# Optimization experiments

Hardware: AMD Instinct MI355X
Metric: run time of the kernel (lower is better)

## Reference

```python
import jax, jax.numpy as jnp
import numpy as np

N_SITE, D, PHYS, W = 40, 128, 2, 8  # sites, MPS bond dim, physical dim, MPO bond dim


def setup_inputs() -> dict:
    key = jax.random.key(0)
    k1, k2 = jax.random.split(key)
    # scale so 40-step transfer-matrix products stay O(1) in float32
    M = jax.random.normal(k1, (N_SITE, D, PHYS, D), jnp.float32) * (D * PHYS) ** -0.5
    H = jax.random.normal(k2, (N_SITE, W, W, PHYS, PHYS), jnp.float32) * (W * PHYS * PHYS) ** -0.5
    return {"M": M, "H": H}


def _energy(M, H):
    # <M|H|M> via left-to-right environment sweep. L has shape (D_bra, w, D_ket).
    L0 = jnp.zeros((D, W, D), M.dtype).at[0, 0, 0].set(1.0)  # open left boundary

    def step(L, mh):
        m, h = mh  # m: (a,i,p) bond,phys,bond ; h: (w,x,i,j) mpo-bond,mpo-bond,phys-out,phys-in
        T = jnp.einsum('awb,aip->wbip', L, m)      # absorb bra tensor (real, so no conj)
        T = jnp.einsum('wbip,wxij->bpxj', T, h)    # absorb MPO tensor
        L = jnp.einsum('bpxj,bjq->pxq', T, m)      # absorb ket tensor
        return L, None

    L, _ = jax.lax.scan(step, L0, (M, H))
    return L[0, W - 1, 0]  # open right boundary (MPO right boundary = last index)


def _norm(M):
    # <M|M> via transfer-matrix sweep. N has shape (D_bra, D_ket); stays PSD.
    N0 = jnp.zeros((D, D), M.dtype).at[0, 0].set(1.0)

    def step(N, m):
        T = jnp.einsum('ab,aip->bip', N, m)
        N = jnp.einsum('bip,biq->pq', T, m)
        return N, None

    N, _ = jax.lax.scan(step, N0, M)
    return N[0, 0]


def reference(M, H):
    EPS = 0.0
    NORM_LIM = 10000.0
    energy = _energy(M, H)
    norm = _norm(M)
    loss = energy / (norm + EPS)  # torch.real is identity for real dtype
    reg = jax.nn.relu(norm - NORM_LIM)
    return (energy, norm, loss, reg)
```

## Files before the change

kernel.cpp:

```cpp
#include <hip/hip_runtime.h>


#define D 128
#define W 8
#define NS 40
#define NPAIR 20
#define HALF2 10
#define MSZ (D * 2 * D)
#define HSZ (W * W * 2 * 2)
#define M2SZ (D * 4 * D)
#define H2SZ (W * W * 4 * 4)
#define LSZ (D * W * D)
#define NSZ (D * D)
#define T2SZ (D * W * D * 4)
#define TNSZ (4 * D * D)

#define OFF_M2 0
#define OFF_MR2 (OFF_M2 + NPAIR * M2SZ)
#define OFF_H2 (OFF_MR2 + HALF2 * M2SZ)
#define OFF_HR2 (OFF_H2 + NPAIR * H2SZ)
#define OFF_LL (OFF_HR2 + HALF2 * H2SZ)
#define OFF_LR (OFF_LL + LSZ)
#define OFF_NL (OFF_LR + LSZ)
#define OFF_NR (OFF_NL + NSZ)
#define OFF_T2L (OFF_NR + NSZ)
#define OFF_T2R (OFF_T2L + T2SZ)
#define OFF_TNL (OFF_T2R + T2SZ)
#define OFF_TNR (OFF_TNL + TNSZ)
#define OFF_PART (OFF_TNR + TNSZ)
#define OFF_PARTN (OFF_PART + 128)

__global__ __launch_bounds__(256) void k_prep1(const float* __restrict__ Min,
                                               const float* __restrict__ Hin,
                                               float* __restrict__ ws) {
    __shared__ float As[32 * 34];
    __shared__ float Bs[32 * 68];
    int bid = blockIdx.x, t = threadIdx.x;
    if (bid < 640) {
        int m = bid >> 5, tile = bid & 31;
        int r0 = (tile & 7) * 32, c0 = (tile >> 3) * 64;
        const float* A = Min + (2 * m) * MSZ;
        const float* B = Min + (2 * m + 1) * MSZ;
        float* C = ws + OFF_M2 + m * M2SZ;
        int ty = t >> 4, tx = t & 15;
        float a00 = 0, a01 = 0, a02 = 0, a03 = 0;
        float a10 = 0, a11 = 0, a12 = 0, a13 = 0;
        for (int c = 0; c < 4; ++c) {
            int k0 = c * 32;
            __syncthreads();
            {
                int rr = t >> 3, kq = t & 7;
                int row = r0 + rr;
                const float4 v = *(const float4*)&A[(row >> 1) * 256 + (row & 1) * 128 + k0 + kq * 4];
                float* dst = &As[kq * 136 + rr];
                dst[0] = v.x; dst[34] = v.y; dst[68] = v.z; dst[102] = v.w;
            }
#pragma unroll
            for (int u = 0; u < 2; ++u) {
                int e = u * 256 + t;
                int kk = e >> 4, cq = e & 15;
                const float4 v = *(const float4*)&B[(k0 + kk) * 256 + c0 + cq * 4];
                *(float4*)&Bs[kk * 68 + cq * 4] = v;
            }
            __syncthreads();
#pragma unroll 8
            for (int kk = 0; kk < 32; ++kk) {
                float2 av = *(float2*)&As[kk * 34 + 2 * ty];
                float4 bv = *(float4*)&Bs[kk * 68 + 4 * tx];
                a00 += av.x * bv.x; a01 += av.x * bv.y; a02 += av.x * bv.z; a03 += av.x * bv.w;
                a10 += av.y * bv.x; a11 += av.y * bv.y; a12 += av.y * bv.z; a13 += av.y * bv.w;
            }
        }
        int r = r0 + 2 * ty, cc = c0 + 4 * tx;
        int a = r >> 1, i2 = cc >> 7, cd = cc & 127;
        float4 v0; v0.x = a00; v0.y = a01; v0.z = a02; v0.w = a03;
        float4 v1; v1.x = a10; v1.y = a11; v1.z = a12; v1.w = a13;
        *(float4*)&C[a * 512 + (0 * 2 + i2) * 128 + cd] = v0;
        *(float4*)&C[a * 512 + (1 * 2 + i2) * 128 + cd] = v1;
    } else {
        for (int idx = t; idx < NPAIR * H2SZ; idx += 256) {
            int m = idx >> 10, r = idx & 1023;
            int w = r >> 7, x = (r >> 4) & 7, I = (r >> 2) & 3, J = r & 3;
            int i1 = I >> 1, i2 = I & 1, j1 = J >> 1, j2 = J & 1;
            const float* Ha = Hin + (2 * m) * HSZ;
            const float* Hb = Hin + (2 * m + 1) * HSZ;
            float s = 0.f;
#pragma unroll
            for (int v = 0; v < 8; ++v)
                s += Ha[w * 32 + v * 4 + i1 * 2 + j1] * Hb[v * 32 + x * 4 + i2 * 2 + j2];
            ws[OFF_H2 + idx] = s;
        }
    }
}

#define PR_MR (HALF2 * M2SZ)
#define PR_HR (PR_MR + HALF2 * H2SZ)
#define PR_TOT (PR_HR + 2 * LSZ + 2 * NSZ)
__global__ __launch_bounds__(256) void k_prep2(float* __restrict__ ws) {
    for (int idx = blockIdx.x * 256 + threadIdx.x; idx < PR_TOT; idx += gridDim.x * 256) {
        if (idx < PR_MR) {
            int kr = idx >> 16, r = idx & 65535;
            int a = r >> 9, I = (r >> 7) & 3, p = r & 127;
            ws[OFF_MR2 + idx] = ws[OFF_M2 + (19 - kr) * M2SZ + p * 512 + I * 128 + a];
        } else if (idx < PR_HR) {
            int e = idx - PR_MR;
            int kr = e >> 10, r = e & 1023;
            int w = r >> 7, x = (r >> 4) & 7, lo = r & 15;
            ws[OFF_HR2 + e] = ws[OFF_H2 + (19 - kr) * H2SZ + x * 128 + w * 16 + lo];
        } else {
            int e = idx - PR_HR;
            int off; float v = 0.f;
            if (e < LSZ)            { off = OFF_LL + e; if (e == 0) v = 1.f; }
            else if (e < 2 * LSZ)   { int r = e - LSZ; off = OFF_LR + r; if (r == (W - 1) * D) v = 1.f; }
            else if (e < 2 * LSZ + NSZ) { int r = e - 2 * LSZ; off = OFF_NL + r; if (r == 0) v = 1.f; }
            else                    { int r = e - 2 * LSZ - NSZ; off = OFF_NR + r; if (r == 0) v = 1.f; }
            ws[off] = v;
        }
    }
}

__global__ __launch_bounds__(512) void k_A2(float* __restrict__ ws, int k) {
    __shared__ __align__(16) float sm[17920];
    int bid = blockIdx.x, t = threadIdx.x;
    int z = t >> 8, tl = t & 255;
    if (bid < 128) {
        int side = bid >> 6;
        int eb = bid & 63;
        int b0 = (eb & 7) * 16;
        int p0 = (eb >> 3) * 16;
        const float* Lsrc = ws + (side ? OFF_LR : OFF_LL);
        const float* m2 = ws + (side ? OFF_MR2 : OFF_M2) + k * M2SZ;
        const float* h2 = ws + (side ? OFF_HR2 : OFF_H2) + k * H2SZ;
        float* T2 = ws + (side ? OFF_T2R : OFF_T2L);
        float* Ls = sm + z * 6400;
        float* ms = sm + 12800 + z * 2048;
        float* hs = sm + 16896;
#pragma unroll
        for (int u = 0; u < 2; ++u) {
            int e = u * 512 + t;
            int w = e >> 7, I = (e >> 5) & 3, x = (e >> 2) & 7, J = e & 3;
            hs[e] = h2[w * 128 + x * 16 + I * 4 + J];
        }
        int b_l = tl & 15, p_l = tl >> 4;
        float acc[8][4];
#pragma unroll
        for (int w = 0; w < 8; ++w)
#pragma unroll
            for (int I = 0; I < 4; ++I) acc[w][I] = 0.f;
        int la[4], lw[4], lb[4], maa[2], mI[2], mpq[2];
#pragma unroll
        for (int u = 0; u < 4; ++u) {
            int e = u * 256 + tl;
            la[u] = e >> 5; lw[u] = (e >> 2) & 7; lb[u] = e & 3;
        }
#pragma unroll
        for (int u = 0; u < 2; ++u) {
            int e = u * 256 + tl;
            maa[u] = e >> 4; mI[u] = (e >> 2) & 3; mpq[u] = e & 3;
        }
        float4 pl[4], pm[2];
        {
            int a0 = z * 64;
#pragma unroll
            for (int u = 0; u < 4; ++u)
                pl[u] = *(const float4*)&Lsrc[(a0 + la[u]) * 1024 + lw[u] * 128 + b0 + lb[u] * 4];
#pragma unroll
            for (int u = 0; u < 2; ++u)
                pm[u] = *(const float4*)&m2[(a0 + maa[u]) * 512 + mI[u] * 128 + p0 + mpq[u] * 4];
        }
        for (int c = 0; c < 2; ++c) {
            __syncthreads();
#pragma unroll
            for (int u = 0; u < 4; ++u) {
                float* dst = &Ls[la[u] * 200 + lb[u] * 48 + lw[u]];
                dst[0] = pl[u].x; dst[12] = pl[u].y; dst[24] = pl[u].z; dst[36] = pl[u].w;
            }
#pragma unroll
            for (int u = 0; u < 2; ++u) {
                int base = maa[u] * 64 + mpq[u] * 16 + mI[u];
                ms[base] = pm[u].x; ms[base + 4] = pm[u].y;
                ms[base + 8] = pm[u].z; ms[base + 12] = pm[u].w;
            }
            if (c == 0) {
                int a0 = z * 64 + 32;
#pragma unroll
                for (int u = 0; u < 4; ++u)
                    pl[u] = *(const float4*)&Lsrc[(a0 + la[u]) * 1024 + lw[u] * 128 + b0 + lb[u] * 4];
#pragma unroll
                for (int u = 0; u < 2; ++u)
                    pm[u] = *(const float4*)&m2[(a0 + maa[u]) * 512 + mI[u] * 128 + p0 + mpq[u] * 4];
            }
            __syncthreads();
#pragma unroll 4
            for (int aa = 0; aa < 32; ++aa) {
                float4 l0 = *(float4*)&Ls[aa * 200 + b_l * 12];
                float4 l1 = *(float4*)&Ls[aa * 200 + b_l * 12 + 4];
                float4 mv = *(float4*)&ms[aa * 64 + p_l * 4];
                float lv[8] = {l0.x, l0.y, l0.z, l0.w, l1.x, l1.y, l1.z, l1.w};
#pragma unroll
                for (int w = 0; w < 8; ++w) {
                    acc[w][0] += lv[w] * mv.x;
                    acc[w][1] += lv[w] * mv.y;
                    acc[w][2] += lv[w] * mv.z;
                    acc[w][3] += lv[w] * mv.w;
                }
            }
        }
        __syncthreads();
        float* red = sm;
        if (z == 1) {
#pragma unroll
            for (int w = 0; w < 8; ++w) {
                float4 v; v.x = acc[w][0]; v.y = acc[w][1]; v.z = acc[w][2]; v.w = acc[w][3];
                *(float4*)&red[tl * 32 + w * 4] = v;
            }
        }
        __syncthreads();
        if (z == 0) {
#pragma unroll
            for (int w = 0; w < 8; ++w) {
                float4 v = *(float4*)&red[tl * 32 + w * 4];
                acc[w][0] += v.x; acc[w][1] += v.y; acc[w][2] += v.z; acc[w][3] += v.w;
            }
            float o[32];
#pragma unroll
            for (int xJ = 0; xJ < 32; ++xJ) o[xJ] = 0.f;
#pragma unroll
            for (int wI = 0; wI < 32; ++wI) {
                float tv = acc[wI >> 2][wI & 3];
#pragma unroll
                for (int xJ = 0; xJ < 32; ++xJ) o[xJ] += tv * hs[wI * 32 + xJ];
            }
            int b = b0 + b_l, p = p0 + p_l;
#pragma unroll
            for (int x = 0; x < 8; ++x) {
                float4 v; v.x = o[x * 4]; v.y = o[x * 4 + 1];
                v.z = o[x * 4 + 2]; v.w = o[x * 4 + 3];
                *(float4*)&T2[p * 4096 + x * 512 + b * 4] = v;
            }
        }
    } else {
        int g = (bid - 128) * 2 + z;
        int side = g >> 5;
        int nn = g & 31;
        int b0 = (nn & 3) * 32;
        int c0 = (nn >> 2) * 64;
        const float* Nsrc = ws + (side ? OFF_NR : OFF_NL);
        const float* m2 = ws + (side ? OFF_MR2 : OFF_M2) + k * M2SZ;
        float* Tn = ws + (side ? OFF_TNR : OFF_TNL);
        float* As = sm + z * 3264;
        float* Bs = sm + z * 3264 + 1056;
        int ty = tl >> 4, tx = tl & 15;
        float a00 = 0, a01 = 0, a02 = 0, a03 = 0;
        float a10 = 0, a11 = 0, a12 = 0, a13 = 0;
        for (int c = 0; c < 4; ++c) {
            int a0 = c * 32;
            __syncthreads();
#pragma unroll
            for (int u = 0; u < 4; ++u) {
                int e = u * 256 + tl;
                int kk = e >> 5, col = e & 31;
                As[kk * 33 + col] = Nsrc[(a0 + kk) * 128 + b0 + col];
            }
#pragma unroll
            for (int u = 0; u < 8; ++u) {
                int e = u * 256 + tl;
                int kk = e >> 6, col = e & 63;
                Bs[kk * 68 + col] = m2[(a0 + kk) * 512 + c0 + col];
            }
            __syncthreads();
#pragma unroll 8
            for (int kk = 0; kk < 32; ++kk) {
                float av0 = As[kk * 33 + 2 * ty], av1 = As[kk * 33 + 2 * ty + 1];
                float4 bv = *(float4*)&Bs[kk * 68 + 4 * tx];
                a00 += av0 * bv.x; a01 += av0 * bv.y; a02 += av0 * bv.z; a03 += av0 * bv.w;
                a10 += av1 * bv.x; a11 += av1 * bv.y; a12 += av1 * bv.z; a13 += av1 * bv.w;
            }
        }
        int b_ = b0 + 2 * ty;
        float rowv[2][4] = {{a00, a01, a02, a03}, {a10, a11, a12, a13}};
#pragma unroll
        for (int jj = 0; jj < 4; ++jj) {
            int col = c0 + 4 * tx + jj;
            int I = col >> 7, p = col & 127;
            Tn[I * 16384 + p * 128 + b_] = rowv[0][jj];
            Tn[I * 16384 + p * 128 + b_ + 1] = rowv[1][jj];
        }
    }
}

__global__ __launch_bounds__(512) void k_B2(float* __restrict__ ws, int k) {
    __shared__ __align__(16) float sm[26624];
    int bid = blockIdx.x, t = threadIdx.x;
    if (bid < 128) {
        int side = bid >> 6;
        int eb = bid & 63;
        int r0 = (eb & 31) * 32;
        int c0 = (eb >> 5) * 64;
        const float* A = ws + (side ? OFF_T2R : OFF_T2L);
        const float* B = ws + (side ? OFF_MR2 : OFF_M2) + k * M2SZ;
        float* C = ws + (side ? OFF_LR : OFF_LL);
        int z = t >> 6, tl = t & 63;
        int ty = tl >> 3, tx = tl & 7;
        float acc[4][8];
#pragma unroll
        for (int j = 0; j < 4; ++j)
#pragma unroll
            for (int q = 0; q < 8; ++q) acc[j][q] = 0.f;
        float* As = sm + z * 3328;
        float* Bs = sm + z * 3328 + 1152;
        int arr[4], akq[4], bkk[8], bcq[8];
#pragma unroll
        for (int u = 0; u < 4; ++u) {
            int e = u * 64 + tl;
            arr[u] = e >> 3; akq[u] = e & 7;
        }
#pragma unroll
        for (int u = 0; u < 8; ++u) {
            int e = u * 64 + tl;
            bkk[u] = e >> 4; bcq[u] = e & 15;
        }
        float4 pa[4], pb[8];
        {
            int k0 = z * 64;
#pragma unroll
            for (int u = 0; u < 4; ++u)
                pa[u] = *(const float4*)&A[(r0 + arr[u]) * 512 + k0 + akq[u] * 4];
#pragma unroll
            for (int u = 0; u < 8; ++u) {
                int row = k0 + bkk[u];
                pb[u] = *(const float4*)&B[(row >> 2) * 512 + (row & 3) * 128 + c0 + bcq[u] * 4];
            }
        }
        for (int c = 0; c < 2; ++c) {
            __syncthreads();
#pragma unroll
            for (int u = 0; u < 4; ++u) {
                float* dst = &As[(akq[u] * 4) * 36 + arr[u]];
                dst[0] = pa[u].x; dst[36] = pa[u].y; dst[72] = pa[u].z; dst[108] = pa[u].w;
            }
#pragma unroll
            for (int u = 0; u < 8; ++u)
                *(float4*)&Bs[bkk[u] * 68 + bcq[u] * 4] = pb[u];
            if (c == 0) {
                int k0 = z * 64 + 32;
#pragma unroll
                for (int u = 0; u < 4; ++u)
                    pa[u] = *(const float4*)&A[(r0 + arr[u]) * 512 + k0 + akq[u] * 4];
#pragma unroll
                for (int u = 0; u < 8; ++u) {
                    int row = k0 + bkk[u];
                    pb[u] = *(const float4*)&B[(row >> 2) * 512 + (row & 3) * 128 + c0 + bcq[u] * 4];
                }
            }
            __syncthreads();
#pragma unroll 8
            for (int kk = 0; kk < 32; ++kk) {
                float4 av = *(float4*)&As[kk * 36 + ty * 4];
                float4 bv0 = *(float4*)&Bs[kk * 68 + tx * 8];
                float4 bv1 = *(float4*)&Bs[kk * 68 + tx * 8 + 4];
                float avv[4] = {av.x, av.y, av.z, av.w};
#pragma unroll
                for (int j = 0; j < 4; ++j) {
                    acc[j][0] += avv[j] * bv0.x; acc[j][1] += avv[j] * bv0.y;
                    acc[j][2] += avv[j] * bv0.z; acc[j][3] += avv[j] * bv0.w;
                    acc[j][4] += avv[j] * bv1.x; acc[j][5] += avv[j] * bv1.y;
                    acc[j][6] += avv[j] * bv1.z; acc[j][7] += avv[j] * bv1.w;
                }
            }
        }
        __syncthreads();
        float* red = sm;
#pragma unroll
        for (int j = 0; j < 4; ++j) {
#pragma unroll
            for (int qq = 0; qq < 2; ++qq) {
                float4 v;
                v.x = acc[j][qq * 4]; v.y = acc[j][qq * 4 + 1];
                v.z = acc[j][qq * 4 + 2]; v.w = acc[j][qq * 4 + 3];
                *(float4*)&red[z * 2048 + tl * 32 + j * 8 + qq * 4] = v;
            }
        }
        __syncthreads();
        {
            int pos = t >> 3;
            int vi0 = (t & 7) * 4;
            float4 s;
            s.x = 0.f; s.y = 0.f; s.z = 0.f; s.w = 0.f;
#pragma unroll
            for (int zz = 0; zz < 8; ++zz) {
                float4 v = *(float4*)&red[zz * 2048 + pos * 32 + vi0];
                s.x += v.x; s.y += v.y; s.z += v.z; s.w += v.w;
            }
            int j = vi0 >> 3;
            int q0 = vi0 & 7;
            int r = r0 + (pos >> 3) * 4 + j;
            int cc = c0 + (pos & 7) * 8 + q0;
            *(float4*)&C[(r >> 3) * 1024 + (r & 7) * 128 + cc] = s;
        }
    } else if (bid < 144) {
        int z = t >> 8, tl = t & 255;
        int ty = tl >> 4, tx = tl & 15;
        float a00 = 0, a01 = 0, a02 = 0, a03 = 0;
        float a10 = 0, a11 = 0, a12 = 0, a13 = 0;
        float* As = sm + z * 3264;
        float* Bs = sm + z * 3264 + 1088;
        float* red = sm + 6528;
        int g = bid - 128;
        int side = g >> 3;
        int nn = g & 7;
        int r0 = (nn & 3) * 32;
        int c0 = (nn >> 2) * 64;
        const float* A = ws + (side ? OFF_TNR : OFF_TNL);
        const float* B = ws + (side ? OFF_MR2 : OFF_M2) + k * M2SZ;
        float* C = ws + (side ? OFF_NR : OFF_NL);
        for (int c = 0; c < 8; ++c) {
            int cg = z * 8 + c;
            int Ic = cg >> 2, bc = (cg & 3) * 32;
            __syncthreads();
            {
                int rr = tl >> 3, kq = tl & 7;
                const float4 v = *(const float4*)&A[Ic * 16384 + (r0 + rr) * 128 + bc + kq * 4];
                float* dst = &As[kq * 136 + rr];
                dst[0] = v.x; dst[34] = v.y; dst[68] = v.z; dst[102] = v.w;
            }
#pragma unroll
            for (int u = 0; u < 2; ++u) {
                int e = u * 256 + tl;
                int kk = e >> 4, cq = e & 15;
                const float4 v = *(const float4*)&B[(bc + kk) * 512 + Ic * 128 + c0 + cq * 4];
                *(float4*)&Bs[kk * 68 + cq * 4] = v;
            }
            __syncthreads();
#pragma unroll 8
            for (int kk = 0; kk < 32; ++kk) {
                float av0 = As[kk * 34 + 2 * ty], av1 = As[kk * 34 + 2 * ty + 1];
                float4 bv = *(float4*)&Bs[kk * 68 + 4 * tx];
                a00 += av0 * bv.x; a01 += av0 * bv.y; a02 += av0 * bv.z; a03 += av0 * bv.w;
                a10 += av1 * bv.x; a11 += av1 * bv.y; a12 += av1 * bv.z; a13 += av1 * bv.w;
            }
        }
        __syncthreads();
        if (z == 1) {
            float4 v0; v0.x = a00; v0.y = a01; v0.z = a02; v0.w = a03;
            float4 v1; v1.x = a10; v1.y = a11; v1.z = a12; v1.w = a13;
            *(float4*)&red[tl * 8] = v0;
            *(float4*)&red[tl * 8 + 4] = v1;
        }
        __syncthreads();
        if (z == 0) {
            float4 v0 = *(float4*)&red[tl * 8];
            float4 v1 = *(float4*)&red[tl * 8 + 4];
            a00 += v0.x; a01 += v0.y; a02 += v0.z; a03 += v0.w;
            a10 += v1.x; a11 += v1.y; a12 += v1.z; a13 += v1.w;
            int r = r0 + 2 * ty, cc = c0 + 4 * tx;
            float4 w0; w0.x = a00; w0.y = a01; w0.z = a02; w0.w = a03;
            float4 w1; w1.x = a10; w1.y = a11; w1.z = a12; w1.w = a13;
            *(float4*)&C[r * 128 + cc] = w0;
            *(float4*)&C[(r + 1) * 128 + cc] = w1;
        }
    }
}

__global__ __launch_bounds__(256) void k_dot(float* __restrict__ ws) {
    __shared__ float se[256], sn[256];
    int bid = blockIdx.x, t = threadIdx.x;
    const float* LL = ws + OFF_LL;
    const float* LR = ws + OFF_LR;
    float e = 0.f;
#pragma unroll
    for (int u = 0; u < 4; ++u) {
        int i = bid * 1024 + u * 256 + t;
        e += LL[i] * LR[i];
    }
    float n = 0.f;
    if (t < 128) {
        int i = bid * 128 + t;
        n = ws[OFF_NL + i] * ws[OFF_NR + i];
    }
    se[t] = e;
    sn[t] = n;
    __syncthreads();
    for (int s = 128; s > 0; s >>= 1) {
        if (t < s) { se[t] += se[t + s]; sn[t] += sn[t + s]; }
        __syncthreads();
    }
    if (t == 0) {
        ws[OFF_PART + bid] = se[0];
        ws[OFF_PARTN + bid] = sn[0];
    }
}

__global__ __launch_bounds__(256) void k_loss(const float* __restrict__ ws,
                                              float* __restrict__ out) {
    __shared__ float se[128], sn[128];
    int t = threadIdx.x;
    if (t < 128) {
        se[t] = ws[OFF_PART + t];
        sn[t] = ws[OFF_PARTN + t];
    }
    __syncthreads();
    for (int s = 64; s > 0; s >>= 1) {
        if (t < s) { se[t] += se[t + s]; sn[t] += sn[t + s]; }
        __syncthreads();
    }
    if (t == 0) {
        float E = se[0], Nm = sn[0];
        out[0] = E;
        out[1] = Nm;
        out[2] = E / Nm;
        out[3] = fmaxf(Nm - 10000.0f, 0.0f);
    }
}

extern "C" void kernel_launch(void* const* d_in, const int* in_sizes, int n_in,
                              void* d_out, int out_size, void* d_ws, size_t ws_size,
                              hipStream_t stream) {
    const float* Min = (const float*)d_in[0];
    const float* Hin = (const float*)d_in[1];
    float* ws = (float*)d_ws;
    float* out = (float*)d_out;
    (void)in_sizes; (void)n_in; (void)out_size; (void)ws_size;

    k_prep1<<<dim3(641), dim3(256), 0, stream>>>(Min, Hin, ws);
    k_prep2<<<dim3(640), dim3(256), 0, stream>>>(ws);
    for (int k = 0; k < HALF2; ++k) {
        k_A2<<<dim3(160), dim3(512), 0, stream>>>(ws, k);
        k_B2<<<dim3(144), dim3(512), 0, stream>>>(ws, k);
    }
    k_dot<<<dim3(128), dim3(256), 0, stream>>>(ws);
    k_loss<<<dim3(1), dim3(256), 0, stream>>>(ws, out);
}
```

Baseline: 429.3 us.

## Rebalance k_B2 split-K: 4 k-slices with 4x4 micro-tiles, unify both branches

The L-environment branch of k_B2 goes from 8 split-K groups with 4x8 per-thread tiles to 4 groups of 128 threads with 4x4 tiles, each looping over four 32-wide k-chunks with register prefetch. The norm branch goes from 2 k-groups with 2x4 tiles to the same 4-group 4x4 layout. The cross-group reduction becomes a simple shared-memory accumulate into group 0, and shared memory drops by half. The aim is to cut the reduction traffic and shared footprint and give more threads per output, at the cost of more serial k-iterations per thread.

```diff
diff --git a/kernel.cpp b/kernel.cpp
--- a/kernel.cpp
+++ b/kernel.cpp
@@ -290,8 +290,17 @@
 }
 
 __global__ __launch_bounds__(512) void k_B2(float* __restrict__ ws, int k) {
-    __shared__ __align__(16) float sm[26624];
+    __shared__ __align__(16) float sm[13312];
     int bid = blockIdx.x, t = threadIdx.x;
+    int z = t >> 7, tl = t & 127;
+    int ty = tl >> 4, tx = tl & 15;
+    float* As = sm + z * 3328;
+    float* Bs = sm + z * 3328 + 1152;
+    float acc[4][4];
+#pragma unroll
+    for (int j = 0; j < 4; ++j)
+#pragma unroll
+        for (int q = 0; q < 4; ++q) acc[j][q] = 0.f;
     if (bid < 128) {
         int side = bid >> 6;
         int eb = bid & 63;
@@ -300,112 +309,83 @@
         const float* A = ws + (side ? OFF_T2R : OFF_T2L);
         const float* B = ws + (side ? OFF_MR2 : OFF_M2) + k * M2SZ;
         float* C = ws + (side ? OFF_LR : OFF_LL);
-        int z = t >> 6, tl = t & 63;
-        int ty = tl >> 3, tx = tl & 7;
-        float acc[4][8];
-#pragma unroll
-        for (int j = 0; j < 4; ++j)
-#pragma unroll
-            for (int q = 0; q < 8; ++q) acc[j][q] = 0.f;
-        float* As = sm + z * 3328;
-        float* Bs = sm + z * 3328 + 1152;
-        int arr[4], akq[4], bkk[8], bcq[8];
-#pragma unroll
-        for (int u = 0; u < 4; ++u) {
-            int e = u * 64 + tl;
-            arr[u] = e >> 3; akq[u] = e & 7;
-        }
-#pragma unroll
-        for (int u = 0; u < 8; ++u) {
-            int e = u * 64 + tl;
-            bkk[u] = e >> 4; bcq[u] = e & 15;
-        }
-        float4 pa[4], pb[8];
+        int arr[2], akq[2], bkk[4], bcq[4];
+#pragma unroll
+        for (int u = 0; u < 2; ++u) { int e = u * 128 + tl; arr[u] = e >> 3; akq[u] = e & 7; }
+#pragma unroll
+        for (int u = 0; u < 4; ++u) { int e = u * 128 + tl; bkk[u] = e >> 4; bcq[u] = e & 15; }
+        float4 pa[2], pb[4];
         {
-            int k0 = z * 64;
-#pragma unroll
-            for (int u = 0; u < 4; ++u)
+            int k0 = (z * 4) * 32;
+#pragma unroll
+            for (int u = 0; u < 2; ++u)
                 pa[u] = *(const float4*)&A[(r0 + arr[u]) * 512 + k0 + akq[u] * 4];
 #pragma unroll
-            for (int u = 0; u < 8; ++u) {
+            for (int u = 0; u < 4; ++u) {
                 int row = k0 + bkk[u];
                 pb[u] = *(const float4*)&B[(row >> 2) * 512 + (row & 3) * 128 + c0 + bcq[u] * 4];
             }
         }
-        for (int c = 0; c < 2; ++c) {
-            __syncthreads();
-#pragma unroll
-            for (int u = 0; u < 4; ++u) {
+        for (int c = 0; c < 4; ++c) {
+            __syncthreads();
+#pragma unroll
+            for (int u = 0; u < 2; ++u) {
                 float* dst = &As[(akq[u] * 4) * 36 + arr[u]];
                 dst[0] = pa[u].x; dst[36] = pa[u].y; dst[72] = pa[u].z; dst[108] = pa[u].w;
             }
 #pragma unroll
-            for (int u = 0; u < 8; ++u)
+            for (int u = 0; u < 4; ++u)
                 *(float4*)&Bs[bkk[u] * 68 + bcq[u] * 4] = pb[u];
-            if (c == 0) {
-                int k0 = z * 64 + 32;
-#pragma unroll
-                for (int u = 0; u < 4; ++u)
-                    pa[u] = *(const float4*)&A[(r0 + arr[u]) * 512 + k0 + akq[u] * 4];
-#pragma unroll
-                for (int u = 0; u < 8; ++u) {
-                    int row = k0 + bkk[u];
+            if (c < 3) {
+                int kn = (z * 4 + c + 1) * 32;
+#pragma unroll
+                for (int u = 0; u < 2; ++u)
+                    pa[u] = *(const float4*)&A[(r0 + arr[u]) * 512 + kn + akq[u] * 4];
+#pragma unroll
+                for (int u = 0; u < 4; ++u) {
+                    int row = kn + bkk[u];
                     pb[u] = *(const float4*)&B[(row >> 2) * 512 + (row & 3) * 128 + c0 + bcq[u] * 4];
                 }
             }
             __syncthreads();
 #pragma unroll 8
             for (int kk = 0; kk < 32; ++kk) {
-                float4 av = *(float4*)&As[kk * 36 + ty * 4];
-                float4 bv0 = *(float4*)&Bs[kk * 68 + tx * 8];
-                float4 bv1 = *(float4*)&Bs[kk * 68 + tx * 8 + 4];
+                float4 av = *(float4*)&As[kk * 36 + 4 * ty];
+                float4 bv = *(float4*)&Bs[kk * 68 + 4 * tx];
                 float avv[4] = {av.x, av.y, av.z, av.w};
 #pragma unroll
                 for (int j = 0; j < 4; ++j) {
-                    acc[j][0] += avv[j] * bv0.x; acc[j][1] += avv[j] * bv0.y;
-                    acc[j][2] += avv[j] * bv0.z; acc[j][3] += avv[j] * bv0.w;
-                    acc[j][4] += avv[j] * bv1.x; acc[j][5] += avv[j] * bv1.y;
-                    acc[j][6] += avv[j] * bv1.z; acc[j][7] += avv[j] * bv1.w;
+                    acc[j][0] += avv[j] * bv.x; acc[j][1] += avv[j] * bv.y;
+                    acc[j][2] += avv[j] * bv.z; acc[j][3] += avv[j] * bv.w;
                 }
             }
         }
         __syncthreads();
-        float* red = sm;
-#pragma unroll
-        for (int j = 0; j < 4; ++j) {
-#pragma unroll
-            for (int qq = 0; qq < 2; ++qq) {
-                float4 v;
-                v.x = acc[j][qq * 4]; v.y = acc[j][qq * 4 + 1];
-                v.z = acc[j][qq * 4 + 2]; v.w = acc[j][qq * 4 + 3];
-                *(float4*)&red[z * 2048 + tl * 32 + j * 8 + qq * 4] = v;
-            }
-        }
-        __syncthreads();
-        {
-            int pos = t >> 3;
-            int vi0 = (t & 7) * 4;
-            float4 s;
-            s.x = 0.f; s.y = 0.f; s.z = 0.f; s.w = 0.f;
-#pragma unroll
-            for (int zz = 0; zz < 8; ++zz) {
-                float4 v = *(float4*)&red[zz * 2048 + pos * 32 + vi0];
-                s.x += v.x; s.y += v.y; s.z += v.z; s.w += v.w;
-            }
-            int j = vi0 >> 3;
-            int q0 = vi0 & 7;
-            int r = r0 + (pos >> 3) * 4 + j;
-            int cc = c0 + (pos & 7) * 8 + q0;
-            *(float4*)&C[(r >> 3) * 1024 + (r & 7) * 128 + cc] = s;
+        if (z != 0) {
+#pragma unroll
+            for (int j = 0; j < 4; ++j) {
+                float4 v; v.x = acc[j][0]; v.y = acc[j][1]; v.z = acc[j][2]; v.w = acc[j][3];
+                *(float4*)&sm[z * 3328 + tl * 16 + j * 4] = v;
+            }
+        }
+        __syncthreads();
+        if (z == 0) {
+#pragma unroll
+            for (int zz = 1; zz < 4; ++zz)
+#pragma unroll
+                for (int j = 0; j < 4; ++j) {
+                    float4 v = *(float4*)&sm[zz * 3328 + tl * 16 + j * 4];
+                    acc[j][0] += v.x; acc[j][1] += v.y; acc[j][2] += v.z; acc[j][3] += v.w;
+                }
+#pragma unroll
+            for (int j = 0; j < 4; ++j) {
+                int r = r0 + 4 * ty + j;
+                int cc = c0 + 4 * tx;
+                float4 v; v.x = acc[j][0]; v.y = acc[j][1]; v.z = acc[j][2]; v.w = acc[j][3];
+                *(float4*)&C[(r >> 3) * 1024 + (r & 7) * 128 + cc] = v;
+            }
         }
     } else if (bid < 144) {
-        int z = t >> 8, tl = t & 255;
-        int ty = tl >> 4, tx = tl & 15;
-        float a00 = 0, a01 = 0, a02 = 0, a03 = 0;
-        float a10 = 0, a11 = 0, a12 = 0, a13 = 0;
-        float* As = sm + z * 3264;
-        float* Bs = sm + z * 3264 + 1088;
-        float* red = sm + 6528;
         int g = bid - 128;
         int side = g >> 3;
         int nn = g & 7;
@@ -414,19 +394,21 @@
         const float* A = ws + (side ? OFF_TNR : OFF_TNL);
         const float* B = ws + (side ? OFF_MR2 : OFF_M2) + k * M2SZ;
         float* C = ws + (side ? OFF_NR : OFF_NL);
-        for (int c = 0; c < 8; ++c) {
-            int cg = z * 8 + c;
+        for (int c = 0; c < 4; ++c) {
+            int cg = z * 4 + c;
             int Ic = cg >> 2, bc = (cg & 3) * 32;
             __syncthreads();
-            {
-                int rr = tl >> 3, kq = tl & 7;
+#pragma unroll
+            for (int u = 0; u < 2; ++u) {
+                int e = u * 128 + tl;
+                int rr = e >> 3, kq = e & 7;
                 const float4 v = *(const float4*)&A[Ic * 16384 + (r0 + rr) * 128 + bc + kq * 4];
-                float* dst = &As[kq * 136 + rr];
-                dst[0] = v.x; dst[34] = v.y; dst[68] = v.z; dst[102] = v.w;
-            }
-#pragma unroll
-            for (int u = 0; u < 2; ++u) {
-                int e = u * 256 + tl;
+                float* dst = &As[(kq * 4) * 36 + rr];
+                dst[0] = v.x; dst[36] = v.y; dst[72] = v.z; dst[108] = v.w;
+            }
+#pragma unroll
+            for (int u = 0; u < 4; ++u) {
+                int e = u * 128 + tl;
                 int kk = e >> 4, cq = e & 15;
                 const float4 v = *(const float4*)&B[(bc + kk) * 512 + Ic * 128 + c0 + cq * 4];
                 *(float4*)&Bs[kk * 68 + cq * 4] = v;
@@ -434,30 +416,40 @@
             __syncthreads();
 #pragma unroll 8
             for (int kk = 0; kk < 32; ++kk) {
-                float av0 = As[kk * 34 + 2 * ty], av1 = As[kk * 34 + 2 * ty + 1];
+                float4 av = *(float4*)&As[kk * 36 + 4 * ty];
                 float4 bv = *(float4*)&Bs[kk * 68 + 4 * tx];
-                a00 += av0 * bv.x; a01 += av0 * bv.y; a02 += av0 * bv.z; a03 += av0 * bv.w;
-                a10 += av1 * bv.x; a11 += av1 * bv.y; a12 += av1 * bv.z; a13 += av1 * bv.w;
-            }
-        }
-        __syncthreads();
-        if (z == 1) {
-            float4 v0; v0.x = a00; v0.y = a01; v0.z = a02; v0.w = a03;
-            float4 v1; v1.x = a10; v1.y = a11; v1.z = a12; v1.w = a13;
-            *(float4*)&red[tl * 8] = v0;
-            *(float4*)&red[tl * 8 + 4] = v1;
+                float avv[4] = {av.x, av.y, av.z, av.w};
+#pragma unroll
+                for (int j = 0; j < 4; ++j) {
+                    acc[j][0] += avv[j] * bv.x; acc[j][1] += avv[j] * bv.y;
+                    acc[j][2] += avv[j] * bv.z; acc[j][3] += avv[j] * bv.w;
+                }
+            }
+        }
+        __syncthreads();
+        if (z != 0) {
+#pragma unroll
+            for (int j = 0; j < 4; ++j) {
+                float4 v; v.x = acc[j][0]; v.y = acc[j][1]; v.z = acc[j][2]; v.w = acc[j][3];
+                *(float4*)&sm[z * 3328 + tl * 16 + j * 4] = v;
+            }
         }
         __syncthreads();
         if (z == 0) {
-            float4 v0 = *(float4*)&red[tl * 8];
-            float4 v1 = *(float4*)&red[tl * 8 + 4];
-            a00 += v0.x; a01 += v0.y; a02 += v0.z; a03 += v0.w;
-            a10 += v1.x; a11 += v1.y; a12 += v1.z; a13 += v1.w;
-            int r = r0 + 2 * ty, cc = c0 + 4 * tx;
-            float4 w0; w0.x = a00; w0.y = a01; w0.z = a02; w0.w = a03;
-            float4 w1; w1.x = a10; w1.y = a11; w1.z = a12; w1.w = a13;
-            *(float4*)&C[r * 128 + cc] = w0;
-            *(float4*)&C[(r + 1) * 128 + cc] = w1;
+#pragma unroll
+            for (int zz = 1; zz < 4; ++zz)
+#pragma unroll
+                for (int j = 0; j < 4; ++j) {
+                    float4 v = *(float4*)&sm[zz * 3328 + tl * 16 + j * 4];
+                    acc[j][0] += v.x; acc[j][1] += v.y; acc[j][2] += v.z; acc[j][3] += v.w;
+                }
+#pragma unroll
+            for (int j = 0; j < 4; ++j) {
+                int r = r0 + 4 * ty + j;
+                int cc = c0 + 4 * tx;
+                float4 v; v.x = acc[j][0]; v.y = acc[j][1]; v.z = acc[j][2]; v.w = acc[j][3];
+                *(float4*)&C[r * 128 + cc] = v;
+            }
         }
     }
 }
```

Result: faster. 417.5 us (-2.7%).
